# Kernel optimization log

Hardware: AMD Instinct MI355X
Metric: run time of the kernel (lower is better)

Reference implementation:

```python
import jax, jax.numpy as jnp
import numpy as np

B, S, H, E, V, OOV = 64, 400, 512, 256, 50000, 100

def setup_inputs() -> dict:
    key = jax.random.key(0)
    ks = jax.random.split(key, 32)
    p = lambda i, shape: jax.random.normal(ks[i], shape, jnp.float32) * 0.02
    emb = p(0, (V, E)).at[0].set(0.0)  # padding_idx=0
    return dict(
        summaries_in=jax.random.randint(ks[1], (B,), 1, V),
        h0=jax.random.normal(ks[2], (B, H), jnp.float32),
        c0=jax.random.normal(ks[3], (B, H), jnp.float32),
        encoder_out=jax.random.normal(ks[4], (B, S, 2 * H), jnp.float32),
        encoder_features=jax.random.normal(ks[5], (S * B, 2 * H), jnp.float32),
        encoder_mask=jnp.ones((S, B), jnp.float32),
        context=jax.random.normal(ks[6], (B, 2 * H), jnp.float32),
        coverage=jax.random.uniform(ks[7], (S, B), jnp.float32) * 0.01,
        texts_extended=jax.random.randint(ks[8], (S, B), 0, V + OOV),
        oov_size=OOV,
        emb=emb,
        W_feat=p(10, (2 * H, 2 * H)), b_feat=p(11, (2 * H,)),
        W_cov=p(12, (2 * H,)), b_cov=p(13, (2 * H,)),
        w_att=p(14, (2 * H,)), b_att=p(15, ()),
        W_ih=p(16, (4 * H, E)), W_hh=p(17, (4 * H, H)),
        b_ih=p(18, (4 * H,)), b_hh=p(19, (4 * H,)),
        W_ctx=p(20, (E, 2 * H + E)), b_ctx=p(21, (E,)),
        W_pg=p(22, (4 * H + E,)), b_pg=p(23, ()),
        W_o1=p(24, (H, 3 * H)), b_o1=p(25, (H,)),
        W_o2=p(26, (V, H)), b_o2=p(27, (V,)),
    )


def reference(summaries_in, h0, c0, encoder_out, encoder_features, encoder_mask,
              context, coverage, texts_extended, oov_size, emb,
              W_feat, b_feat, W_cov, b_cov, w_att, b_att,
              W_ih, W_hh, b_ih, b_hh, W_ctx, b_ctx, W_pg, b_pg,
              W_o1, b_o1, W_o2, b_o2):
    # embedding + context projection: [B, 2H+E] -> [B, E]
    x = emb[summaries_in]
    ctx_out = jnp.concatenate([context, x], axis=1) @ W_ctx.T + b_ctx
    # single LSTM step (torch gate order i, f, g, o)
    gates = ctx_out @ W_ih.T + b_ih + h0 @ W_hh.T + b_hh
    i, f, g, o = jnp.split(gates, 4, axis=1)
    c = jax.nn.sigmoid(f) * c0 + jax.nn.sigmoid(i) * jnp.tanh(g)
    h = jax.nn.sigmoid(o) * jnp.tanh(c)
    hidden_out = jnp.concatenate([h, c], axis=1)  # [B, 2H]
    # Bahdanau attention with coverage
    dec_feat = hidden_out @ W_feat.T + b_feat                 # [B, 2H]
    ef = encoder_features.reshape(S, B, 2 * H)                # [S, B, 2H]
    cov_feat = coverage[..., None] * W_cov + b_cov            # Linear(1, 2H)
    e = jnp.tanh(ef + dec_feat[None] + cov_feat) @ w_att + b_att  # [S, B]
    a = jax.nn.softmax(e, axis=0) * encoder_mask
    a = a / jnp.sum(a, axis=0, keepdims=True)                 # renormalize (Normalize(0))
    ctx_new = jnp.einsum('sb,bsd->bd', a, encoder_out)        # [B, 2H]
    coverage_next = coverage + a
    # pointer-generator mix
    gen_in = jnp.concatenate([ctx_new, hidden_out, ctx_out], axis=1)  # [B, 4H+E]
    p_gen = jax.nn.sigmoid(gen_in @ W_pg + b_pg)[:, None]             # [B, 1]
    logits = (jnp.concatenate([h, ctx_new], axis=1) @ W_o1.T + b_o1) @ W_o2.T + b_o2
    vocab_dist = p_gen * jax.nn.softmax(logits, axis=1)       # [B, V]
    attn_w = (1.0 - p_gen) * a.T                              # [B, S]
    vd = jnp.concatenate([vocab_dist, jnp.zeros((B, oov_size), vocab_dist.dtype)], axis=1)
    vd = vd.at[jnp.arange(B)[:, None], texts_extended.T].add(attn_w)  # scatter_add copy dist
    return vd, hidden_out, ctx_new, a, coverage_next
```

## Files before the change

### kernel.cpp

```cpp
#include <hip/hip_runtime.h>
#include <cmath>

#define B 64
#define S 400
#define H 512
#define E 256
#define V 50000
#define OOV 100
#define H2 1024
#define VDN (V + OOV)
#define NBLK_V 782
#define SC 8

typedef __attribute__((ext_vector_type(8))) short short8;
typedef __attribute__((ext_vector_type(4))) float f32x4;

__device__ __forceinline__ float wred_sum(float v) {
#pragma unroll
  for (int o = 32; o > 0; o >>= 1) v += __shfl_down(v, o, 64);
  return v;
}
__device__ __forceinline__ float wred_max(float v) {
#pragma unroll
  for (int o = 32; o > 0; o >>= 1) v = fmaxf(v, __shfl_down(v, o, 64));
  return v;
}
__device__ __forceinline__ short f2bf(float f) {
  return __builtin_bit_cast(short, (__bf16)f);
}
__device__ __forceinline__ float bf2f(unsigned short u) {
  unsigned x = (unsigned)u << 16;
  return __builtin_bit_cast(float, x);
}
__device__ __forceinline__ float ftanh(float x) {
  float e = __expf(2.f * x);
  return 1.f - 2.f * __builtin_amdgcn_rcpf(e + 1.f);
}
__device__ __forceinline__ float fsig(float x) {
  return __builtin_amdgcn_rcpf(1.f + __expf(-x));
}

__global__ __launch_bounds__(256) void k_pre(
    const float* __restrict__ b_ctx, const float* __restrict__ b_ih,
    const float* __restrict__ b_hh, const float* __restrict__ b_feat,
    const float* __restrict__ b_o1, const float* __restrict__ context,
    const float* __restrict__ emb, const int* __restrict__ sumin,
    const float* __restrict__ h0, float* __restrict__ ctxoutT4,
    float* __restrict__ gates, float* __restrict__ dfeat,
    float* __restrict__ innerT4, float* __restrict__ catT4,
    float* __restrict__ h0T4, float* __restrict__ Zb) {
  int idx = blockIdx.x * 256 + threadIdx.x;
  if (idx < 64) Zb[idx] = 0.f;
  if (idx < 16384) {
    int j = ((idx >> 8) << 2) + (idx & 3);
    ctxoutT4[idx] = b_ctx[j];
  } else if (idx < 16384 + 131072) {
    int i = idx - 16384;
    int j = i & 2047;
    gates[i] = b_ih[j] + b_hh[j];
  } else if (idx < 16384 + 131072 + 65536) {
    int i = idx - 16384 - 131072;
    dfeat[i] = b_feat[i & 1023];
  } else if (idx < 245760) {
    int i = idx - 16384 - 131072 - 65536;
    int j = ((i >> 8) << 2) + (i & 3);
    innerT4[i] = b_o1[j];
  } else if (idx < 245760 + 81920) {
    int i = idx - 245760;
    int e = i & 3, b = (i >> 2) & 63, q = i >> 8;
    int k = q * 4 + e;
    catT4[i] = (k < 1024) ? context[b * 1024 + k]
                          : emb[(size_t)sumin[b] * 256 + (k - 1024)];
  } else {
    int i = idx - 245760 - 81920;
    int e = i & 3, b = (i >> 2) & 63, q = i >> 8;
    h0T4[i] = h0[b * 512 + q * 4 + e];
  }
}

template <int R, int KC, int OUTMODE>
__global__ __launch_bounds__(256) void k_gemmsk(
    const float* __restrict__ A1, const float* __restrict__ W1, int ldw1, int s1,
    const float* __restrict__ A2, const float* __restrict__ W2, int ldw2,
    float* __restrict__ out, int ldout) {
  const int lane = threadIdx.x;
  const int w = threadIdx.y;
  const int j0 = blockIdx.x * (4 * R) + w * R;
  const float* A;
  const float* W;
  int ldw, kc0;
  if ((int)blockIdx.y < s1) {
    A = A1; W = W1; ldw = ldw1; kc0 = blockIdx.y * KC;
  } else {
    A = A2; W = W2; ldw = ldw2; kc0 = (blockIdx.y - s1) * KC;
  }
  float acc[R];
#pragma unroll
  for (int r = 0; r < R; ++r) acc[r] = 0.f;
  const float* ap = A + (size_t)kc0 * 256 + lane * 4;
  const float* wr[R];
#pragma unroll
  for (int r = 0; r < R; ++r) wr[r] = W + (size_t)(j0 + r) * ldw + kc0 * 4;
#pragma unroll 8
  for (int k4 = 0; k4 < KC; ++k4) {
    float4 av = *(const float4*)(ap + (size_t)k4 * 256);
#pragma unroll
    for (int r = 0; r < R; ++r) {
      float4 wv = *(const float4*)(wr[r] + k4 * 4);
      acc[r] += av.x * wv.x + av.y * wv.y + av.z * wv.z + av.w * wv.w;
    }
  }
#pragma unroll
  for (int r = 0; r < R; ++r) {
    int j = j0 + r;
    if constexpr (OUTMODE == 0)
      atomicAdd(&out[((size_t)(j >> 2) * 64 + lane) * 4 + (j & 3)], acc[r]);
    else
      atomicAdd(&out[(size_t)lane * ldout + j], acc[r]);
  }
}

__global__ __launch_bounds__(256) void k_lstm(const float* __restrict__ gates,
                                              const float* __restrict__ c0,
                                              float* __restrict__ hidden,
                                              float* __restrict__ hcT4) {
  int idx = blockIdx.x * 256 + threadIdx.x;
  int b = idx >> 9, u = idx & 511;
  float gi = gates[(size_t)b * 2048 + u];
  float gf = gates[(size_t)b * 2048 + 512 + u];
  float gg = gates[(size_t)b * 2048 + 1024 + u];
  float go = gates[(size_t)b * 2048 + 1536 + u];
  float c = fsig(gf) * c0[(size_t)b * 512 + u] + fsig(gi) * ftanh(gg);
  float h = fsig(go) * ftanh(c);
  hidden[(size_t)b * H2 + u] = h;
  hidden[(size_t)b * H2 + 512 + u] = c;
  hcT4[((u >> 2) * 64 + b) * 4 + (u & 3)] = h;
  int k = 512 + u;
  hcT4[((k >> 2) * 64 + b) * 4 + (k & 3)] = c;
}

__global__ __launch_bounds__(256) void k_e(
    const float* __restrict__ ef, const float* __restrict__ dfeat,
    const float* __restrict__ cov, const float* __restrict__ Wcov,
    const float* __restrict__ bcov, const float* __restrict__ watt,
    const float* __restrict__ batt, const float* __restrict__ mask,
    float* __restrict__ e_x, float* __restrict__ Zb) {
  const int t = threadIdx.x;
  const int b = blockIdx.x & 63;
  const int q = blockIdx.x >> 6;
  float4 dv = ((const float4*)(dfeat + (size_t)b * H2))[t];
  float4 bc = ((const float4*)bcov)[t];
  float4 wc = ((const float4*)Wcov)[t];
  float4 wa = ((const float4*)watt)[t];
  const float bx = dv.x + bc.x, by = dv.y + bc.y;
  const float bz = dv.z + bc.z, bw = dv.w + bc.w;
  float4 evs[8];
  float cvals[8];
#pragma unroll
  for (int i = 0; i < 8; ++i) {
    const int sb = (q * 8 + i) * B + b;
    evs[i] = ((const float4*)(ef + (size_t)sb * H2))[t];
    cvals[i] = cov[sb];
  }
  __shared__ float part[8][4];
#pragma unroll
  for (int i = 0; i < 8; ++i) {
    float sum = ftanh(evs[i].x + bx + cvals[i] * wc.x) * wa.x +
                ftanh(evs[i].y + by + cvals[i] * wc.y) * wa.y +
                ftanh(evs[i].z + bz + cvals[i] * wc.z) * wa.z +
                ftanh(evs[i].w + bw + cvals[i] * wc.w) * wa.w;
    sum = wred_sum(sum);
    if ((t & 63) == 0) part[i][t >> 6] = sum;
  }
  __syncthreads();
  if (t < 64) {
    float x = 0.f;
    if (t < 8) {
      int sb = (q * 8 + t) * B + b;
      float e = part[t][0] + part[t][1] + part[t][2] + part[t][3] + batt[0];
      x = mask[sb] * __expf(e);
      e_x[sb] = x;
    }
#pragma unroll
    for (int o = 4; o > 0; o >>= 1) x += __shfl_down(x, o, 64);
    if (t == 0) atomicAdd(&Zb[b], x);
  }
}

__global__ __launch_bounds__(256) void k_softctx(
    const float* __restrict__ e_x, const float* __restrict__ Zb,
    const float* __restrict__ coverage, const float* __restrict__ enc,
    float* __restrict__ a_out, float* __restrict__ cov_out,
    float* __restrict__ part) {
  const int b = blockIdx.x & 63;
  const int sc = blockIdx.x >> 6;
  const int t = threadIdx.x;
  __shared__ float aS[50];
  const float rZ = 1.f / Zb[b];
  if (t < 50) {
    int s = sc * 50 + t;
    int sb = s * B + b;
    float av = e_x[sb] * rZ;
    aS[t] = av;
    a_out[sb] = av;
    cov_out[sb] = coverage[sb] + av;
  }
  __syncthreads();
  const int d = t * 4;
  float4 acc = make_float4(0.f, 0.f, 0.f, 0.f);
#pragma unroll 10
  for (int i = 0; i < 50; ++i) {
    int s = sc * 50 + i;
    float av = aS[i];
    float4 ev = *(const float4*)(enc + ((size_t)b * S + s) * H2 + d);
    acc.x += av * ev.x;
    acc.y += av * ev.y;
    acc.z += av * ev.z;
    acc.w += av * ev.w;
  }
  *(float4*)(part + (size_t)blockIdx.x * H2 + d) = acc;
}

__global__ __launch_bounds__(256) void k_ctxpg(
    const float* __restrict__ part, const float* __restrict__ hidden,
    const float* __restrict__ ctxoutT4, const float* __restrict__ Wpg,
    const float* __restrict__ bpg, float* __restrict__ ctx_new,
    float* __restrict__ ctxT4, float* __restrict__ pgen) {
  const int b = blockIdx.x;
  const int t = threadIdx.x;
  const int lane = t & 63, w = t >> 6;
  const int d = t * 4;
  float4 s = make_float4(0.f, 0.f, 0.f, 0.f);
#pragma unroll
  for (int sc = 0; sc < SC; ++sc) {
    float4 v = *(const float4*)(part + (size_t)(sc * 64 + b) * H2 + d);
    s.x += v.x; s.y += v.y; s.z += v.z; s.w += v.w;
  }
  *(float4*)(ctx_new + (size_t)b * H2 + d) = s;
  *(float4*)(ctxT4 + (size_t)t * 256 + b * 4) = s;
  float p = s.x * Wpg[d] + s.y * Wpg[d + 1] + s.z * Wpg[d + 2] + s.w * Wpg[d + 3];
#pragma unroll
  for (int j = 0; j < 4; ++j) {
    int k = t + j * 256;
    p += hidden[(size_t)b * H2 + k] * Wpg[1024 + k];
  }
  p += ctxoutT4[(size_t)(t >> 2) * 256 + b * 4 + (t & 3)] * Wpg[2048 + t];
  p = wred_sum(p);
  __shared__ float red[4];
  if (lane == 0) red[w] = p;
  __syncthreads();
  if (t == 0) {
    float dd = red[0] + red[1] + red[2] + red[3] + bpg[0];
    pgen[b] = fsig(dd);
  }
}

__global__ __launch_bounds__(256) void k_packinner(const float* __restrict__ innerT4,
                                                   short8* __restrict__ packB) {
  int f = blockIdx.x * 256 + threadIdx.x;
  int l = f & 63, bt = (f >> 6) & 3, ks = f >> 8;
  int b = bt * 16 + (l & 15);
  int kbase = ks * 32 + (l >> 4) * 8;
  float4 q0 = *(const float4*)&innerT4[(size_t)(kbase / 4) * 256 + b * 4];
  float4 q1 = *(const float4*)&innerT4[(size_t)(kbase / 4 + 1) * 256 + b * 4];
  short8 frag;
  frag[0] = f2bf(q0.x); frag[1] = f2bf(q0.y);
  frag[2] = f2bf(q0.z); frag[3] = f2bf(q0.w);
  frag[4] = f2bf(q1.x); frag[5] = f2bf(q1.y);
  frag[6] = f2bf(q1.z); frag[7] = f2bf(q1.w);
  packB[f] = frag;
}

__global__ __launch_bounds__(256) void k_mfma_logits(
    const float* __restrict__ W2, const short8* __restrict__ packB,
    const float* __restrict__ bias, unsigned short* __restrict__ logits_bf,
    float* __restrict__ mp, float* __restrict__ zp) {
  const int l = threadIdx.x;
  const int w = threadIdx.y;
  const int jblk = blockIdx.x * 64;
  const int jv = min(jblk + w * 16 + (l & 15), V - 1);
  const float4* wp4 = (const float4*)(W2 + (size_t)jv * 512 + (l >> 4) * 8);

  f32x4 acc0 = {0.f, 0.f, 0.f, 0.f}, acc1 = acc0, acc2 = acc0, acc3 = acc0;
  float4 cw0 = wp4[0], cw1 = wp4[1];
#pragma unroll
  for (int ks = 0; ks < 16; ++ks) {
    float4 nw0, nw1;
    if (ks < 15) { nw0 = wp4[(ks + 1) * 8]; nw1 = wp4[(ks + 1) * 8 + 1]; }
    short8 af;
    af[0] = f2bf(cw0.x); af[1] = f2bf(cw0.y); af[2] = f2bf(cw0.z); af[3] = f2bf(cw0.w);
    af[4] = f2bf(cw1.x); af[5] = f2bf(cw1.y); af[6] = f2bf(cw1.z); af[7] = f2bf(cw1.w);
    short8 b0 = packB[(ks * 4 + 0) * 64 + l];
    short8 b1 = packB[(ks * 4 + 1) * 64 + l];
    short8 b2 = packB[(ks * 4 + 2) * 64 + l];
    short8 b3 = packB[(ks * 4 + 3) * 64 + l];
    acc0 = __builtin_amdgcn_mfma_f32_16x16x32_bf16(af, b0, acc0, 0, 0, 0);
    acc1 = __builtin_amdgcn_mfma_f32_16x16x32_bf16(af, b1, acc1, 0, 0, 0);
    acc2 = __builtin_amdgcn_mfma_f32_16x16x32_bf16(af, b2, acc2, 0, 0, 0);
    acc3 = __builtin_amdgcn_mfma_f32_16x16x32_bf16(af, b3, acc3, 0, 0, 0);
    if (ks < 15) { cw0 = nw0; cw1 = nw1; }
  }

  __shared__ float tile[64][65];
  const int rbase = w * 16 + (l >> 4) * 4;
#pragma unroll
  for (int v = 0; v < 4; ++v) {
    int jl = rbase + v;
    int j = jblk + jl;
    float bv = bias[min(j, V - 1)];
    bool valid = (j < V);
    tile[jl][0 * 16 + (l & 15)] = valid ? acc0[v] + bv : -INFINITY;
    tile[jl][1 * 16 + (l & 15)] = valid ? acc1[v] + bv : -INFINITY;
    tile[jl][2 * 16 + (l & 15)] = valid ? acc2[v] + bv : -INFINITY;
    tile[jl][3 * 16 + (l & 15)] = valid ? acc3[v] + bv : -INFINITY;
  }
  __syncthreads();
  const int t = w * 64 + l;
#pragma unroll
  for (int i = 0; i < 16; ++i) {
    int idx = i * 256 + t;
    int jl = idx & 63;
    int b = idx >> 6;
    int j = jblk + jl;
    if (j < V)
      logits_bf[(size_t)b * V + j] = (unsigned short)f2bf(tile[jl][b]);
  }
  if (t < 64) {
    float m = -INFINITY;
#pragma unroll
    for (int jl = 0; jl < 64; ++jl) m = fmaxf(m, tile[jl][t]);
    float z = 0.f;
#pragma unroll
    for (int jl = 0; jl < 64; ++jl) z += __expf(tile[jl][t] - m);
    mp[(size_t)blockIdx.x * 64 + t] = m;
    zp[(size_t)blockIdx.x * 64 + t] = z;
  }
}

__global__ __launch_bounds__(256) void k_vdms(
    const unsigned short* __restrict__ logits_bf, const float* __restrict__ mp,
    const float* __restrict__ zp, const float* __restrict__ pgen,
    const float* __restrict__ a_out, const int* __restrict__ tex,
    float* __restrict__ out) {
  const int b = blockIdx.x >> 3;
  const int c = blockIdx.x & 7;
  const int t = threadIdx.x;
  const int lane = t & 63, w = t >> 6;
  __shared__ float red[4];
  __shared__ float hist[6272];
  float m = -INFINITY;
  for (int i = t; i < NBLK_V; i += 256) m = fmaxf(m, mp[i * 64 + b]);
  m = wred_max(m);
  if (lane == 0) red[w] = m;
  __syncthreads();
  const float M = fmaxf(fmaxf(red[0], red[1]), fmaxf(red[2], red[3]));
  __syncthreads();
  float z = 0.f;
  for (int i = t; i < NBLK_V; i += 256) z += zp[i * 64 + b] * __expf(mp[i * 64 + b] - M);
  z = wred_sum(z);
  if (lane == 0) red[w] = z;
  __syncthreads();
  const float Z = red[0] + red[1] + red[2] + red[3];
  const float pg = pgen[b];
  const float scale = pg / Z;
  const float wq = 1.f - pg;
  const int v0 = c * 6272;
  const int v1 = min(v0 + 6272, VDN);
  for (int i = t; i < 6272; i += 256) hist[i] = 0.f;
  __syncthreads();
  for (int s = t; s < S; s += 256) {
    int v = tex[s * B + b];
    if (v >= v0 && v < v1) atomicAdd(&hist[v - v0], wq * a_out[s * B + b]);
  }
  __syncthreads();
  for (int v = v0 + t; v < v1; v += 256) {
    float val =
        (v < V) ? scale * __expf(bf2f(logits_bf[(size_t)b * V + v]) - M) : 0.f;
    out[(size_t)b * VDN + v] = val + hist[v - v0];
  }
}

extern "C" void kernel_launch(void* const* d_in, const int* in_sizes, int n_in,
                              void* d_out, int out_size, void* d_ws, size_t ws_size,
                              hipStream_t stream) {
  const int* sumin = (const int*)d_in[0];
  const float* h0 = (const float*)d_in[1];
  const float* c0 = (const float*)d_in[2];
  const float* enc_out = (const float*)d_in[3];
  const float* ef = (const float*)d_in[4];
  const float* mask = (const float*)d_in[5];
  const float* context = (const float*)d_in[6];
  const float* coverage = (const float*)d_in[7];
  const int* tex = (const int*)d_in[8];
  const float* emb = (const float*)d_in[10];
  const float* W_feat = (const float*)d_in[11];
  const float* b_feat = (const float*)d_in[12];
  const float* W_cov = (const float*)d_in[13];
  const float* b_cov = (const float*)d_in[14];
  const float* w_att = (const float*)d_in[15];
  const float* b_att = (const float*)d_in[16];
  const float* W_ih = (const float*)d_in[17];
  const float* W_hh = (const float*)d_in[18];
  const float* b_ih = (const float*)d_in[19];
  const float* b_hh = (const float*)d_in[20];
  const float* W_ctx = (const float*)d_in[21];
  const float* b_ctx = (const float*)d_in[22];
  const float* W_pg = (const float*)d_in[23];
  const float* b_pg = (const float*)d_in[24];
  const float* W_o1 = (const float*)d_in[25];
  const float* b_o1 = (const float*)d_in[26];
  const float* W_o2 = (const float*)d_in[27];
  const float* b_o2 = (const float*)d_in[28];

  float* out = (float*)d_out;
  float* vd = out;
  float* hidden = vd + (size_t)B * VDN;
  float* ctx_new = hidden + (size_t)B * H2;
  float* a_out = ctx_new + (size_t)B * H2;
  float* cov_out = a_out + (size_t)S * B;

  float* ws = (float*)d_ws;
  float* catT4 = ws;
  float* h0T4 = catT4 + 81920;
  float* ctxoutT4 = h0T4 + 32768;
  float* gates = ctxoutT4 + 16384;
  float* hidcatT4 = gates + 131072;
  float* dfeat = hidcatT4 + 65536;
  float* e_x = dfeat + 65536;
  float* ctxnewT4 = e_x + 25600;
  float* innerT4 = ctxnewT4 + 65536;
  float* pgen = innerT4 + 32768;
  float* Zb = pgen + 64;
  float* mp = Zb + 64;
  float* zp = mp + 50048;
  float* packBf = zp + 50048;
  float* logits = packBf + 16384;
  float* part = logits + 1600064;
  short8* packB = (short8*)packBf;
  unsigned short* logits_bf = (unsigned short*)logits;

  dim3 gblk(64, 4);

  k_pre<<<1408, 256, 0, stream>>>(b_ctx, b_ih, b_hh, b_feat, b_o1, context, emb,
                                  sumin, h0, ctxoutT4, gates, dfeat, innerT4,
                                  catT4, h0T4, Zb);
  k_gemmsk<2, 64, 0><<<dim3(32, 5), gblk, 0, stream>>>(
      catT4, W_ctx, 1280, 5, nullptr, nullptr, 0, ctxoutT4, 0);
  k_gemmsk<2, 64, 1><<<dim3(256, 3), gblk, 0, stream>>>(
      ctxoutT4, W_ih, 256, 1, h0T4, W_hh, 512, gates, 2048);
  k_lstm<<<128, 256, 0, stream>>>(gates, c0, hidden, hidcatT4);
  k_gemmsk<2, 64, 1><<<dim3(128, 4), gblk, 0, stream>>>(
      hidcatT4, W_feat, 1024, 4, nullptr, nullptr, 0, dfeat, 1024);
  k_e<<<50 * 64, 256, 0, stream>>>(ef, dfeat, coverage, W_cov, b_cov, w_att,
                                   b_att, mask, e_x, Zb);
  k_softctx<<<SC * B, 256, 0, stream>>>(e_x, Zb, coverage, enc_out, a_out,
                                        cov_out, part);
  k_ctxpg<<<B, 256, 0, stream>>>(part, hidden, ctxoutT4, W_pg, b_pg, ctx_new,
                                 ctxnewT4, pgen);
  k_gemmsk<2, 64, 0><<<dim3(64, 6), gblk, 0, stream>>>(
      hidcatT4, W_o1, 1536, 2, ctxnewT4, W_o1 + 512, 1536, innerT4, 0);
  k_packinner<<<16, 256, 0, stream>>>(innerT4, packB);
  k_mfma_logits<<<NBLK_V, gblk, 0, stream>>>(W_o2, packB, b_o2, logits_bf, mp, zp);
  k_vdms<<<B * 8, 256, 0, stream>>>(logits_bf, mp, zp, pgen, a_out, tex, vd);
}
```

Measured before the change: 211.3 us.

## Fuse attention context accumulation into score kernel with deferred softmax normalization

The attention score kernel now also loads the matching encoder_out rows and accumulates unnormalized exp-weighted context partials per 8-position chunk. The separate softmax/context kernel is removed: the final reduce kernel sums the partials, scales by 1/Z, and writes the attention and coverage outputs. This saves a launch and spreads the encoder_out read across many more blocks. In exchange it writes and re-reads many more per-chunk partials (50 chunks instead of 8), and that reduction runs on only 64 blocks.

```diff
diff --git a/kernel.cpp b/kernel.cpp
--- a/kernel.cpp
+++ b/kernel.cpp
@@ -10,7 +10,7 @@
 #define H2 1024
 #define VDN (V + OOV)
 #define NBLK_V 782
-#define SC 8
+#define SC 50
 
 typedef __attribute__((ext_vector_type(8))) short short8;
 typedef __attribute__((ext_vector_type(4))) float f32x4;
@@ -139,12 +139,13 @@
   hcT4[((k >> 2) * 64 + b) * 4 + (k & 3)] = c;
 }
 
-__global__ __launch_bounds__(256) void k_e(
+__global__ __launch_bounds__(256) void k_ectx(
     const float* __restrict__ ef, const float* __restrict__ dfeat,
     const float* __restrict__ cov, const float* __restrict__ Wcov,
     const float* __restrict__ bcov, const float* __restrict__ watt,
     const float* __restrict__ batt, const float* __restrict__ mask,
-    float* __restrict__ e_x, float* __restrict__ Zb) {
+    const float* __restrict__ enc, float* __restrict__ e_x,
+    float* __restrict__ Zb, float* __restrict__ partc) {
   const int t = threadIdx.x;
   const int b = blockIdx.x & 63;
   const int q = blockIdx.x >> 6;
@@ -154,15 +155,17 @@
   float4 wa = ((const float4*)watt)[t];
   const float bx = dv.x + bc.x, by = dv.y + bc.y;
   const float bz = dv.z + bc.z, bw = dv.w + bc.w;
-  float4 evs[8];
+  float4 evs[8], encs[8];
   float cvals[8];
 #pragma unroll
   for (int i = 0; i < 8; ++i) {
-    const int sb = (q * 8 + i) * B + b;
-    evs[i] = ((const float4*)(ef + (size_t)sb * H2))[t];
-    cvals[i] = cov[sb];
-  }
-  __shared__ float part[8][4];
+    const int s = q * 8 + i;
+    evs[i] = ((const float4*)(ef + (size_t)(s * B + b) * H2))[t];
+    encs[i] = ((const float4*)(enc + ((size_t)b * S + s) * H2))[t];
+    cvals[i] = cov[s * B + b];
+  }
+  __shared__ float ered[8][4];
+  __shared__ float xS[8];
 #pragma unroll
   for (int i = 0; i < 8; ++i) {
     float sum = ftanh(evs[i].x + bx + cvals[i] * wc.x) * wa.x +
@@ -170,74 +173,67 @@
                 ftanh(evs[i].z + bz + cvals[i] * wc.z) * wa.z +
                 ftanh(evs[i].w + bw + cvals[i] * wc.w) * wa.w;
     sum = wred_sum(sum);
-    if ((t & 63) == 0) part[i][t >> 6] = sum;
+    if ((t & 63) == 0) ered[i][t >> 6] = sum;
   }
   __syncthreads();
   if (t < 64) {
     float x = 0.f;
     if (t < 8) {
       int sb = (q * 8 + t) * B + b;
-      float e = part[t][0] + part[t][1] + part[t][2] + part[t][3] + batt[0];
+      float e = ered[t][0] + ered[t][1] + ered[t][2] + ered[t][3] + batt[0];
       x = mask[sb] * __expf(e);
       e_x[sb] = x;
+      xS[t] = x;
     }
 #pragma unroll
     for (int o = 4; o > 0; o >>= 1) x += __shfl_down(x, o, 64);
     if (t == 0) atomicAdd(&Zb[b], x);
   }
-}
-
-__global__ __launch_bounds__(256) void k_softctx(
-    const float* __restrict__ e_x, const float* __restrict__ Zb,
-    const float* __restrict__ coverage, const float* __restrict__ enc,
-    float* __restrict__ a_out, float* __restrict__ cov_out,
-    float* __restrict__ part) {
-  const int b = blockIdx.x & 63;
-  const int sc = blockIdx.x >> 6;
-  const int t = threadIdx.x;
-  __shared__ float aS[50];
-  const float rZ = 1.f / Zb[b];
-  if (t < 50) {
-    int s = sc * 50 + t;
-    int sb = s * B + b;
-    float av = e_x[sb] * rZ;
-    aS[t] = av;
-    a_out[sb] = av;
-    cov_out[sb] = coverage[sb] + av;
-  }
-  __syncthreads();
-  const int d = t * 4;
+  __syncthreads();
   float4 acc = make_float4(0.f, 0.f, 0.f, 0.f);
-#pragma unroll 10
-  for (int i = 0; i < 50; ++i) {
-    int s = sc * 50 + i;
-    float av = aS[i];
-    float4 ev = *(const float4*)(enc + ((size_t)b * S + s) * H2 + d);
-    acc.x += av * ev.x;
-    acc.y += av * ev.y;
-    acc.z += av * ev.z;
-    acc.w += av * ev.w;
-  }
-  *(float4*)(part + (size_t)blockIdx.x * H2 + d) = acc;
+#pragma unroll
+  for (int i = 0; i < 8; ++i) {
+    float x = xS[i];
+    acc.x += x * encs[i].x;
+    acc.y += x * encs[i].y;
+    acc.z += x * encs[i].z;
+    acc.w += x * encs[i].w;
+  }
+  ((float4*)(partc + (size_t)blockIdx.x * H2))[t] = acc;
 }
 
 __global__ __launch_bounds__(256) void k_ctxpg(
-    const float* __restrict__ part, const float* __restrict__ hidden,
-    const float* __restrict__ ctxoutT4, const float* __restrict__ Wpg,
-    const float* __restrict__ bpg, float* __restrict__ ctx_new,
-    float* __restrict__ ctxT4, float* __restrict__ pgen) {
+    const float* __restrict__ partc, const float* __restrict__ e_x,
+    const float* __restrict__ Zb, const float* __restrict__ coverage,
+    const float* __restrict__ hidden, const float* __restrict__ ctxoutT4,
+    const float* __restrict__ Wpg, const float* __restrict__ bpg,
+    float* __restrict__ ctx_new, float* __restrict__ ctxT4,
+    float* __restrict__ pgen, float* __restrict__ a_out,
+    float* __restrict__ cov_out) {
   const int b = blockIdx.x;
   const int t = threadIdx.x;
   const int lane = t & 63, w = t >> 6;
+  const float rZ = 1.f / Zb[b];
   const int d = t * 4;
   float4 s = make_float4(0.f, 0.f, 0.f, 0.f);
-#pragma unroll
+#pragma unroll 10
   for (int sc = 0; sc < SC; ++sc) {
-    float4 v = *(const float4*)(part + (size_t)(sc * 64 + b) * H2 + d);
+    float4 v = *(const float4*)(partc + (size_t)(sc * 64 + b) * H2 + d);
     s.x += v.x; s.y += v.y; s.z += v.z; s.w += v.w;
   }
+  s.x *= rZ; s.y *= rZ; s.z *= rZ; s.w *= rZ;
   *(float4*)(ctx_new + (size_t)b * H2 + d) = s;
   *(float4*)(ctxT4 + (size_t)t * 256 + b * 4) = s;
+#pragma unroll
+  for (int i = 0; i < 2; ++i) {
+    int sidx = t + i * 256;
+    if (sidx < S) {
+      int sb = sidx * B + b;
+      float av = e_x[sb] * rZ;
+      a_out[sb] = av;
+      cov_out[sb] = coverage[sb] + av;
+    }
+  }
   float p = s.x * Wpg[d] + s.y * Wpg[d + 1] + s.z * Wpg[d + 2] + s.w * Wpg[d + 3];
 #pragma unroll
   for (int j = 0; j < 4; ++j) {
@@ -435,7 +431,7 @@
   float* zp = mp + 50048;
   float* packBf = zp + 50048;
   float* logits = packBf + 16384;
-  float* part = logits + 1600064;
+  float* partc = logits + 1600064;
   short8* packB = (short8*)packBf;
   unsigned short* logits_bf = (unsigned short*)logits;
 
@@ -451,12 +447,11 @@
   k_lstm<<<128, 256, 0, stream>>>(gates, c0, hidden, hidcatT4);
   k_gemmsk<2, 64, 1><<<dim3(128, 4), gblk, 0, stream>>>(
       hidcatT4, W_feat, 1024, 4, nullptr, nullptr, 0, dfeat, 1024);
-  k_e<<<50 * 64, 256, 0, stream>>>(ef, dfeat, coverage, W_cov, b_cov, w_att,
-                                   b_att, mask, e_x, Zb);
-  k_softctx<<<SC * B, 256, 0, stream>>>(e_x, Zb, coverage, enc_out, a_out,
-                                        cov_out, part);
-  k_ctxpg<<<B, 256, 0, stream>>>(part, hidden, ctxoutT4, W_pg, b_pg, ctx_new,
-                                 ctxnewT4, pgen);
+  k_ectx<<<SC * B, 256, 0, stream>>>(ef, dfeat, coverage, W_cov, b_cov, w_att,
+                                     b_att, mask, enc_out, e_x, Zb, partc);
+  k_ctxpg<<<B, 256, 0, stream>>>(partc, e_x, Zb, coverage, hidden, ctxoutT4,
+                                 W_pg, b_pg, ctx_new, ctxnewT4, pgen, a_out,
+                                 cov_out);
   k_gemmsk<2, 64, 0><<<dim3(64, 6), gblk, 0, stream>>>(
       hidcatT4, W_o1, 1536, 2, ctxnewT4, W_o1 + 512, 1536, innerT4, 0);
   k_packinner<<<16, 256, 0, stream>>>(innerT4, packB);
```

Result: faster. 207.1 us (-2.0%).
